# Optimization experiments

Hardware: AMD Instinct MI355X
Metric: run time of the kernel (lower is better)

## Reference

```python
import jax, jax.numpy as jnp
import numpy as np

N_NODES = 100000
N_EDGES = 1600000
IN_C = 128
HID = 128
OUT_C = 10
N_GRAPHS = 512


def setup_inputs() -> dict:
    key = jax.random.key(0)
    ks = jax.random.split(key, 12)
    x = jax.random.normal(ks[0], (N_NODES, IN_C), dtype=jnp.float32)
    edge_index = jax.random.randint(ks[1], (2, N_EDGES), 0, N_NODES, dtype=jnp.int64)
    batch = jnp.sort(jax.random.randint(ks[2], (N_NODES,), 0, N_GRAPHS, dtype=jnp.int64))

    def lin(k, fan_in, fan_out):
        bound = 1.0 / np.sqrt(fan_in)
        return jax.random.uniform(k, (fan_in, fan_out), jnp.float32, -bound, bound)

    params = {
        # GraphConv layer i: W_rel (neighbor aggregate transform, with bias),
        # W_root (self transform, no bias) -- matches PyG GraphConv.
        "W1_rel": lin(ks[3], IN_C, HID), "b1": jnp.zeros((HID,), jnp.float32), "W1_root": lin(ks[4], IN_C, HID),
        "W2_rel": lin(ks[5], HID, HID), "b2": jnp.zeros((HID,), jnp.float32), "W2_root": lin(ks[6], HID, HID),
        "W3_rel": lin(ks[7], HID, HID), "b3": jnp.zeros((HID,), jnp.float32), "W3_root": lin(ks[8], HID, HID),
        "W_lin": lin(ks[9], HID, OUT_C), "b_lin": jnp.zeros((OUT_C,), jnp.float32),
    }
    return {"x": x, "edge_index": edge_index, "batch": batch, **params}


def _graph_conv(x, src, dst, W_rel, b, W_root):
    # PyG GraphConv with aggr='add': out_i = W_rel @ sum_{j->i} x_j + b + W_root @ x_i
    agg = jax.ops.segment_sum(x[src], dst, num_segments=x.shape[0])  # [N, d]
    return agg @ W_rel + b + x @ W_root


def reference(x, edge_index, batch,
              W1_rel, b1, W1_root,
              W2_rel, b2, W2_root,
              W3_rel, b3, W3_root,
              W_lin, b_lin):
    src, dst = edge_index[0], edge_index[1]
    h = jax.nn.relu(_graph_conv(x, src, dst, W1_rel, b1, W1_root))
    h = jax.nn.relu(_graph_conv(h, src, dst, W2_rel, b2, W2_root))
    h = _graph_conv(h, src, dst, W3_rel, b3, W3_root)
    # global mean pool over graphs
    sums = jax.ops.segment_sum(h, batch, num_segments=N_GRAPHS)             # [G, d]
    counts = jax.ops.segment_sum(jnp.ones((h.shape[0],), h.dtype), batch, num_segments=N_GRAPHS)
    pooled = sums / jnp.maximum(counts, 1.0)[:, None]
    return pooled @ W_lin + b_lin  # [G, OUT_C]
```

## Files before the change

### kernel.cpp

```cpp
#include <hip/hip_runtime.h>

static constexpr int NN = 100000;
static constexpr int NE = 1600000;
static constexpr int C  = 128;
static constexpr int OC = 10;
static constexpr int NG = 512;

static constexpr int BSH  = 9;
static constexpr int BNW  = 1 << BSH;
static constexpr int BK   = (NN + BNW - 1) / BNW;
static constexpr int BCAP = 12288;
static constexpr int EPB  = 4096;
static constexpr int ABLK = (NE + EPB - 1) / EPB;

static constexpr int TSTRIDE = 132;
static constexpr int NSPLIT = 8;

static constexpr int PB_PACK = BK;
static constexpr int PB_GB   = PB_PACK + 16;
static constexpr int PB_WF   = PB_GB + 2;
static constexpr int PB_CVT  = PB_WF + 5;
static constexpr int PB_TOT  = PB_CVT + (NN * C / 8 + 511) / 512;

typedef unsigned short u16;
typedef __attribute__((ext_vector_type(8))) short short8;
typedef __attribute__((ext_vector_type(8))) short bf16x8;
typedef __attribute__((ext_vector_type(4))) float f32x4;

__device__ __forceinline__ float bf2f(u16 u) {
    union { float f; unsigned int u32; } v; v.u32 = ((unsigned int)u) << 16; return v.f;
}
__device__ __forceinline__ u16 f2bf(float f) {
    union { float f; unsigned int u; } v; v.f = f;
    unsigned int u = v.u;
    unsigned int r = u + 0x7FFF + ((u >> 16) & 1);
    return (u16)(r >> 16);
}

__global__ __launch_bounds__(256) void k_binA(const int* __restrict__ src,
                                              const int* __restrict__ dst,
                                              int* __restrict__ gcnt,
                                              int* __restrict__ buck) {
    __shared__ int cnt[BK];
    __shared__ int curs[BK];
    int tid = threadIdx.x;
    for (int i = tid; i < BK; i += 256) cnt[i] = 0;
    __syncthreads();
    int e0 = blockIdx.x * EPB;
    for (int i = tid; i < EPB; i += 256) {
        int e = e0 + i;
        if (e < NE) atomicAdd(&cnt[dst[e] >> BSH], 1);
    }
    __syncthreads();
    for (int i = tid; i < BK; i += 256) {
        int c = cnt[i];
        int gb = (c > 0) ? atomicAdd(&gcnt[i], c) : 0;
        curs[i] = i * BCAP + gb;
    }
    __syncthreads();
    for (int i = tid; i < EPB; i += 256) {
        int e = e0 + i;
        if (e < NE) {
            int d = dst[e];
            int b = d >> BSH;
            int p = atomicAdd(&curs[b], 1);
            if (p < (b + 1) * BCAP)
                buck[p] = (src[e] << BSH) | (d & (BNW - 1));
        }
    }
}

__global__ __launch_bounds__(512) void k_binbprep(
    const int* __restrict__ gcnt, const int* __restrict__ buck,
    int* __restrict__ rp, int* __restrict__ csr,
    const float* __restrict__ x, u16* __restrict__ xb,
    const float* __restrict__ W1r, const float* __restrict__ W1o,
    const float* __restrict__ W2r, const float* __restrict__ W2o,
    u16* __restrict__ Bp,
    const int* __restrict__ batch, int* __restrict__ gstart,
    const float* __restrict__ W3r, const float* __restrict__ W3o,
    const float* __restrict__ b3, const float* __restrict__ W_lin,
    const float* __restrict__ b_lin,
    float* __restrict__ Wrl, float* __restrict__ Wro, float* __restrict__ bfold) {
    int bid = blockIdx.x;
    int tid = threadIdx.x;

    if (bid < BK) {
        __shared__ int hist[BNW];
        __shared__ int scanbuf[BNW];
        int b = bid;

        scanbuf[tid] = (tid < b) ? gcnt[tid] : 0;
        __syncthreads();
        for (int off = 1; off < BNW; off <<= 1) {
            int t = (tid >= off) ? scanbuf[tid - off] : 0;
            __syncthreads();
            scanbuf[tid] += t;
            __syncthreads();
        }
        int base = scanbuf[BNW - 1];

        int n = gcnt[b];
        if (n > BCAP) n = BCAP;
        const int* bb = buck + (size_t)b * BCAP;

        hist[tid] = 0;
        __syncthreads();
        for (int i = tid; i < n; i += BNW) atomicAdd(&hist[bb[i] & (BNW - 1)], 1);
        __syncthreads();

        int v = hist[tid];
        scanbuf[tid] = v;
        __syncthreads();
        for (int off = 1; off < BNW; off <<= 1) {
            int t = (tid >= off) ? scanbuf[tid - off] : 0;
            __syncthreads();
            scanbuf[tid] += t;
            __syncthreads();
        }
        int excl = scanbuf[tid] - v;
        int node = (b << BSH) + tid;
        if (node < NN) rp[node] = base + excl;
        if (b == 0 && tid == 0) rp[NN] = NE;
        __syncthreads();
        hist[tid] = base + excl;
        __syncthreads();
        for (int i = tid; i < n; i += BNW) {
            int en = bb[i];
            int p = atomicAdd(&hist[en & (BNW - 1)], 1);
            csr[p] = en >> BSH;
        }
    } else if (bid < PB_GB) {
        int tt = (bid - PB_PACK) * 512 + tid;
        int layer = tt >> 12;
        int t = tt & 4095;
        const float* Wr = (layer == 0) ? W1r : W2r;
        const float* Wo = (layer == 0) ? W1o : W2o;
        u16* outp = Bp + layer * 32768;
        int lane = t & 63;
        int nfrag = (t >> 6) & 7;
        int kk = t >> 9;
        int col = nfrag * 16 + (lane & 15);
        int k0 = kk * 32 + (lane >> 4) * 8;
        u16 vals[8];
#pragma unroll
        for (int j = 0; j < 8; ++j) {
            int k = k0 + j;
            float w = (k < C) ? Wr[k * C + col] : Wo[(k - C) * C + col];
            vals[j] = f2bf(w);
        }
        *reinterpret_cast<short8*>(outp + (size_t)t * 8) = *reinterpret_cast<const short8*>(vals);
    } else if (bid < PB_WF) {
        int g = (bid - PB_GB) * 512 + tid;
        if (g > NG) return;
        int lo = 0, hi = NN;
        while (lo < hi) { int mid = (lo + hi) >> 1; if (batch[mid] < g) lo = mid + 1; else hi = mid; }
        gstart[g] = lo;
    } else if (bid < PB_CVT) {
        int idx = (bid - PB_WF) * 512 + tid;
        if (idx >= OC * 256) return;
        int o = idx >> 8;
        int sub = idx & 255;
        if (sub < 128) {
            float s = 0.0f;
#pragma unroll 8
            for (int c = 0; c < C; ++c) s += W3r[sub * C + c] * W_lin[c * OC + o];
            Wrl[sub * OC + o] = s;
        } else {
            int k = sub - 128;
            float s = 0.0f;
#pragma unroll 8
            for (int c = 0; c < C; ++c) s += W3o[k * C + c] * W_lin[c * OC + o];
            Wro[k * OC + o] = s;
        }
        if (sub == 0) {
            float s = 0.0f;
            for (int c = 0; c < C; ++c) s += b3[c] * W_lin[c * OC + o];
            bfold[o] = b_lin[o] + s;
        }
    } else {
        int i = (bid - PB_CVT) * 512 + tid;
        size_t base = (size_t)i * 8;
        if (base >= (size_t)NN * C) return;
        float4 a = *reinterpret_cast<const float4*>(x + base);
        float4 b = *reinterpret_cast<const float4*>(x + base + 4);
        u16 o[8] = { f2bf(a.x), f2bf(a.y), f2bf(a.z), f2bf(a.w),
                     f2bf(b.x), f2bf(b.y), f2bf(b.z), f2bf(b.w) };
        *reinterpret_cast<short8*>(xb + base) = *reinterpret_cast<const short8*>(o);
    }
}

__global__ __launch_bounds__(256) void k_gather(const u16* __restrict__ h,
                                                const int* __restrict__ rp,
                                                const int* __restrict__ csr,
                                                u16* __restrict__ agg) {
    int t = blockIdx.x * blockDim.x + threadIdx.x;
    int node = t >> 6;
    if (node >= NN) return;
    int lane = t & 63;
    int jj = lane >> 4;
    int seg = (lane & 15) * 8;
    int beg = rp[node], end = rp[node + 1];

    float acc[8] = {};
    int j0 = beg;
    for (; j0 + 8 <= end; j0 += 8) {
        int sa = csr[j0 + jj];
        int sb = csr[j0 + 4 + jj];
        short8 va = *reinterpret_cast<const short8*>(h + (size_t)sa * C + seg);
        short8 vb = *reinterpret_cast<const short8*>(h + (size_t)sb * C + seg);
#pragma unroll
        for (int q = 0; q < 8; ++q) {
            acc[q] += bf2f((u16)va[q]);
            acc[q] += bf2f((u16)vb[q]);
        }
    }
    if (j0 < end) {
        int ja = j0 + jj;
        int jb = j0 + 4 + jj;
        if (ja < end) {
            int sa = csr[ja];
            short8 va = *reinterpret_cast<const short8*>(h + (size_t)sa * C + seg);
#pragma unroll
            for (int q = 0; q < 8; ++q) acc[q] += bf2f((u16)va[q]);
        }
        if (jb < end) {
            int sb = csr[jb];
            short8 vb = *reinterpret_cast<const short8*>(h + (size_t)sb * C + seg);
#pragma unroll
            for (int q = 0; q < 8; ++q) acc[q] += bf2f((u16)vb[q]);
        }
    }

#pragma unroll
    for (int q = 0; q < 8; ++q) {
        acc[q] += __shfl_xor(acc[q], 32);
        acc[q] += __shfl_xor(acc[q], 16);
    }
    if (lane < 16) {
        u16 o[8];
#pragma unroll
        for (int q = 0; q < 8; ++q) o[q] = f2bf(acc[q]);
        *reinterpret_cast<short8*>(agg + (size_t)node * C + seg) =
            *reinterpret_cast<const short8*>(o);
    }
}

template <bool RELU, bool TSUM>
__global__ __launch_bounds__(256) void k_transform_mfma(
    const u16* __restrict__ agg, const u16* __restrict__ h,
    const u16* __restrict__ Bp, const float* __restrict__ bias,
    u16* __restrict__ out,
    const int* __restrict__ batch, float* __restrict__ Tpart) {
    __shared__ u16 tile[4][16 * TSTRIDE];
    int wave = threadIdx.x >> 6;
    int lane = threadIdx.x & 63;
    int row0 = blockIdx.x * 64 + wave * 16;
    int arow = row0 + (lane & 15);
    int rclamp = arow < NN ? arow : NN - 1;
    int koff = (lane >> 4) * 8;

    bf16x8 afr[8];
#pragma unroll
    for (int kk = 0; kk < 4; ++kk)
        afr[kk] = *reinterpret_cast<const bf16x8*>(agg + (size_t)rclamp * C + kk * 32 + koff);
#pragma unroll
    for (int kk = 0; kk < 4; ++kk)
        afr[4 + kk] = *reinterpret_cast<const bf16x8*>(h + (size_t)rclamp * C + kk * 32 + koff);

    f32x4 acc[8] = {};
#pragma unroll
    for (int kk = 0; kk < 8; ++kk) {
        const u16* bp = Bp + ((size_t)kk * 8 * 64 + lane) * 8;
#pragma unroll
        for (int n = 0; n < 8; ++n) {
            bf16x8 b = *reinterpret_cast<const bf16x8*>(bp + (size_t)n * 64 * 8);
            acc[n] = __builtin_amdgcn_mfma_f32_16x16x32_bf16(afr[kk], b, acc[n], 0, 0, 0);
        }
    }

    u16* T = tile[wave];
    int colbase = lane & 15;
    int rloc = (lane >> 4) * 4;
#pragma unroll
    for (int n = 0; n < 8; ++n) {
        int col = n * 16 + colbase;
        float bb = bias[col];
#pragma unroll
        for (int r = 0; r < 4; ++r) {
            float v = acc[n][r] + bb;
            if (RELU) v = fmaxf(v, 0.0f);
            T[(rloc + r) * TSTRIDE + col] = f2bf(v);
        }
    }
    __syncthreads();

#pragma unroll
    for (int k = 0; k < 4; ++k) {
        int idx = k * 64 + lane;
        int lr = idx >> 4;
        int off = (idx & 15) * 8;
        int ro = row0 + lr;
        if (ro < NN) {
            short8 v = *reinterpret_cast<const short8*>(&T[lr * TSTRIDE + off]);
            *reinterpret_cast<short8*>(out + (size_t)ro * C + off) = v;
        }
    }

    if (TSUM) {
        if (threadIdx.x < C) {
            int c = threadIdx.x;
            int base = blockIdx.x * 64;
            float run = 0.0f;
            int curg = -1;
            for (int r = 0; r < 64; ++r) {
                int ro = base + r;
                if (ro >= NN) break;
                int g = batch[ro];
                if (g != curg) {
                    if (curg >= 0) atomicAdd(&Tpart[(size_t)curg * C + c], run);
                    run = 0.0f;
                    curg = g;
                }
                run += bf2f(tile[r >> 4][(r & 15) * TSTRIDE + c]);
            }
            if (curg >= 0) atomicAdd(&Tpart[(size_t)curg * C + c], run);
        }
    }
}

__global__ __launch_bounds__(256) void k_gsum(
    const u16* __restrict__ h, const int* __restrict__ rp,
    const int* __restrict__ csr, const int* __restrict__ gstart,
    float* __restrict__ partial) {
    int b = blockIdx.x;
    int g = b >> 3;
    int p = b & 7;
    int slot = threadIdx.x >> 4;
    int seg = (threadIdx.x & 15) * 8;

    int gs = gstart[g], ge = gstart[g + 1];
    int es = rp[gs], ee = rp[ge];
    int m = ee - es;
    int js = es + (int)(((long long)m * p) >> 3);
    int je = es + (int)(((long long)m * (p + 1)) >> 3);

    float acc[8] = {};
    int j = js + slot;
    for (; j + 48 < je; j += 64) {
        int r0 = csr[j];
        int r1 = csr[j + 16];
        int r2 = csr[j + 32];
        int r3 = csr[j + 48];
        short8 v0 = *reinterpret_cast<const short8*>(h + (size_t)r0 * C + seg);
        short8 v1 = *reinterpret_cast<const short8*>(h + (size_t)r1 * C + seg);
        short8 v2 = *reinterpret_cast<const short8*>(h + (size_t)r2 * C + seg);
        short8 v3 = *reinterpret_cast<const short8*>(h + (size_t)r3 * C + seg);
#pragma unroll
        for (int q = 0; q < 8; ++q) {
            acc[q] += bf2f((u16)v0[q]);
            acc[q] += bf2f((u16)v1[q]);
            acc[q] += bf2f((u16)v2[q]);
            acc[q] += bf2f((u16)v3[q]);
        }
    }
    for (; j < je; j += 16) {
        int r0 = csr[j];
        short8 v0 = *reinterpret_cast<const short8*>(h + (size_t)r0 * C + seg);
#pragma unroll
        for (int q = 0; q < 8; ++q) acc[q] += bf2f((u16)v0[q]);
    }

    __shared__ float red[16][C];
#pragma unroll
    for (int q = 0; q < 8; ++q) red[slot][seg + q] = acc[q];
    __syncthreads();
    if (threadIdx.x < C) {
        float s = 0.0f;
#pragma unroll
        for (int r = 0; r < 16; ++r) s += red[r][threadIdx.x];
        partial[(size_t)b * C + threadIdx.x] = s;
    }
}

__global__ __launch_bounds__(128) void k_gout(
    const float* __restrict__ partial, const float* __restrict__ Tpart,
    const int* __restrict__ gstart,
    const float* __restrict__ Wrl, const float* __restrict__ Wro,
    const float* __restrict__ bfold, float* __restrict__ out) {
    int g = blockIdx.x;
    int k = threadIdx.x;
    __shared__ float S[C], T[C];
    float s = 0.0f;
#pragma unroll
    for (int p = 0; p < NSPLIT; ++p)
        s += partial[((size_t)(g * NSPLIT + p)) * C + k];
    S[k] = s;
    T[k] = Tpart[(size_t)g * C + k];
    __syncthreads();
    if (k < OC) {
        int n = gstart[g + 1] - gstart[g];
        float inv = 1.0f / (float)max(n, 1);
        float o = bfold[k];
#pragma unroll 8
        for (int kk = 0; kk < C; ++kk)
            o += (S[kk] * Wrl[kk * OC + k] + T[kk] * Wro[kk * OC + k]) * inv;
        out[g * OC + k] = o;
    }
}

extern "C" void kernel_launch(void* const* d_in, const int* in_sizes, int n_in,
                              void* d_out, int out_size, void* d_ws, size_t ws_size,
                              hipStream_t stream) {
    const float* x       = (const float*)d_in[0];
    const int*   eidx    = (const int*)d_in[1];
    const int*   batch   = (const int*)d_in[2];
    const float* W1_rel  = (const float*)d_in[3];
    const float* b1      = (const float*)d_in[4];
    const float* W1_root = (const float*)d_in[5];
    const float* W2_rel  = (const float*)d_in[6];
    const float* b2      = (const float*)d_in[7];
    const float* W2_root = (const float*)d_in[8];
    const float* W3_rel  = (const float*)d_in[9];
    const float* b3      = (const float*)d_in[10];
    const float* W3_root = (const float*)d_in[11];
    const float* W_lin   = (const float*)d_in[12];
    const float* b_lin   = (const float*)d_in[13];
    float* out = (float*)d_out;

    const int* src = eidx;
    const int* dst = eidx + NE;

    u16* xb   = (u16*)d_ws;
    u16* hb   = xb + (size_t)NN * C;
    u16* aggb = hb + (size_t)NN * C;
    u16* Bp   = aggb + (size_t)NN * C;
    int* rp      = (int*)(Bp + 2 * 32768);
    int* csr     = rp + NN + 1;
    int* buck    = csr + NE;
    int* gcnt    = buck + (size_t)BK * BCAP;
    float* Tpart = (float*)(gcnt + BK);
    int* gstart  = (int*)(Tpart + (size_t)NG * C);
    float* partial = (float*)(gstart + NG + 2);
    float* Wrl   = partial + (size_t)NG * NSPLIT * C;
    float* Wro   = Wrl + C * OC;
    float* bfold = Wro + C * OC;

    const int gb = (NN * 64 + 255) / 256;
    const int tb = (NN + 63) / 64;

    hipMemsetAsync(gcnt, 0, BK * sizeof(int) + (size_t)NG * C * sizeof(float), stream);
    k_binA<<<ABLK, 256, 0, stream>>>(src, dst, gcnt, buck);

    k_binbprep<<<PB_TOT, 512, 0, stream>>>(gcnt, buck, rp, csr,
                                           x, xb, W1_rel, W1_root, W2_rel, W2_root,
                                           Bp, batch, gstart,
                                           W3_rel, W3_root, b3, W_lin, b_lin,
                                           Wrl, Wro, bfold);

    k_gather<<<gb, 256, 0, stream>>>(xb, rp, csr, aggb);
    k_transform_mfma<true, false><<<tb, 256, 0, stream>>>(aggb, xb, Bp, b1, hb,
                                                          batch, Tpart);

    k_gather<<<gb, 256, 0, stream>>>(hb, rp, csr, aggb);
    k_transform_mfma<true, true><<<tb, 256, 0, stream>>>(aggb, hb, Bp + 32768, b2,
                                                         hb, batch, Tpart);

    k_gsum<<<NG * NSPLIT, 256, 0, stream>>>(hb, rp, csr, gstart, partial);
    k_gout<<<NG, 128, 0, stream>>>(partial, Tpart, gstart, Wrl, Wro, bfold, out);
}
```

Baseline: 294.8 us.

## Regroup prep kernels, stage weight fragments in LDS, fuse graph output into gsum

Moves the weight packing, x-to-bf16 conversion and graph-start search into the edge-binning kernel, and runs the CSR build as its own kernel. The MFMA transform now double-buffers the packed weight fragments through shared memory instead of reading them from global memory per wave. The final per-graph projection is folded into the gsum kernel using a last-block atomic counter, which removes one launch. This adds extra barriers in the transform loop and a fence-plus-atomic step at the end of every gsum block.

Result: slower. 899.1 us (+205.0%).

```diff
diff --git a/kernel.cpp b/kernel.cpp
--- a/kernel.cpp
+++ b/kernel.cpp
@@ -16,11 +16,11 @@
 static constexpr int TSTRIDE = 132;
 static constexpr int NSPLIT = 8;
 
-static constexpr int PB_PACK = BK;
-static constexpr int PB_GB   = PB_PACK + 16;
-static constexpr int PB_WF   = PB_GB + 2;
-static constexpr int PB_CVT  = PB_WF + 5;
-static constexpr int PB_TOT  = PB_CVT + (NN * C / 8 + 511) / 512;
+static constexpr int APB_PACK = ABLK;
+static constexpr int APB_GB   = APB_PACK + 32;
+static constexpr int APB_WF   = APB_GB + 3;
+static constexpr int APB_CVT  = APB_WF + 10;
+static constexpr int APB_TOT  = APB_CVT + (NN * C / 8 + 255) / 256;
 
 typedef unsigned short u16;
 typedef __attribute__((ext_vector_type(8))) short short8;
@@ -37,42 +37,9 @@
     return (u16)(r >> 16);
 }
 
-__global__ __launch_bounds__(256) void k_binA(const int* __restrict__ src,
-                                              const int* __restrict__ dst,
-                                              int* __restrict__ gcnt,
-                                              int* __restrict__ buck) {
-    __shared__ int cnt[BK];
-    __shared__ int curs[BK];
-    int tid = threadIdx.x;
-    for (int i = tid; i < BK; i += 256) cnt[i] = 0;
-    __syncthreads();
-    int e0 = blockIdx.x * EPB;
-    for (int i = tid; i < EPB; i += 256) {
-        int e = e0 + i;
-        if (e < NE) atomicAdd(&cnt[dst[e] >> BSH], 1);
-    }
-    __syncthreads();
-    for (int i = tid; i < BK; i += 256) {
-        int c = cnt[i];
-        int gb = (c > 0) ? atomicAdd(&gcnt[i], c) : 0;
-        curs[i] = i * BCAP + gb;
-    }
-    __syncthreads();
-    for (int i = tid; i < EPB; i += 256) {
-        int e = e0 + i;
-        if (e < NE) {
-            int d = dst[e];
-            int b = d >> BSH;
-            int p = atomicAdd(&curs[b], 1);
-            if (p < (b + 1) * BCAP)
-                buck[p] = (src[e] << BSH) | (d & (BNW - 1));
-        }
-    }
-}
-
-__global__ __launch_bounds__(512) void k_binbprep(
-    const int* __restrict__ gcnt, const int* __restrict__ buck,
-    int* __restrict__ rp, int* __restrict__ csr,
+__global__ __launch_bounds__(256) void k_binA_prep(
+    const int* __restrict__ src, const int* __restrict__ dst,
+    int* __restrict__ gcnt, int* __restrict__ buck,
     const float* __restrict__ x, u16* __restrict__ xb,
     const float* __restrict__ W1r, const float* __restrict__ W1o,
     const float* __restrict__ W2r, const float* __restrict__ W2o,
@@ -85,53 +52,35 @@
     int bid = blockIdx.x;
     int tid = threadIdx.x;
 
-    if (bid < BK) {
-        __shared__ int hist[BNW];
-        __shared__ int scanbuf[BNW];
-        int b = bid;
-
-        scanbuf[tid] = (tid < b) ? gcnt[tid] : 0;
-        __syncthreads();
-        for (int off = 1; off < BNW; off <<= 1) {
-            int t = (tid >= off) ? scanbuf[tid - off] : 0;
-            __syncthreads();
-            scanbuf[tid] += t;
-            __syncthreads();
-        }
-        int base = scanbuf[BNW - 1];
-
-        int n = gcnt[b];
-        if (n > BCAP) n = BCAP;
-        const int* bb = buck + (size_t)b * BCAP;
-
-        hist[tid] = 0;
-        __syncthreads();
-        for (int i = tid; i < n; i += BNW) atomicAdd(&hist[bb[i] & (BNW - 1)], 1);
-        __syncthreads();
-
-        int v = hist[tid];
-        scanbuf[tid] = v;
-        __syncthreads();
-        for (int off = 1; off < BNW; off <<= 1) {
-            int t = (tid >= off) ? scanbuf[tid - off] : 0;
-            __syncthreads();
-            scanbuf[tid] += t;
-            __syncthreads();
-        }
-        int excl = scanbuf[tid] - v;
-        int node = (b << BSH) + tid;
-        if (node < NN) rp[node] = base + excl;
-        if (b == 0 && tid == 0) rp[NN] = NE;
-        __syncthreads();
-        hist[tid] = base + excl;
-        __syncthreads();
-        for (int i = tid; i < n; i += BNW) {
-            int en = bb[i];
-            int p = atomicAdd(&hist[en & (BNW - 1)], 1);
-            csr[p] = en >> BSH;
-        }
-    } else if (bid < PB_GB) {
-        int tt = (bid - PB_PACK) * 512 + tid;
+    if (bid < ABLK) {
+        __shared__ int cnt[BK];
+        __shared__ int curs[BK];
+        for (int i = tid; i < BK; i += 256) cnt[i] = 0;
+        __syncthreads();
+        int e0 = bid * EPB;
+        for (int i = tid; i < EPB; i += 256) {
+            int e = e0 + i;
+            if (e < NE) atomicAdd(&cnt[dst[e] >> BSH], 1);
+        }
+        __syncthreads();
+        for (int i = tid; i < BK; i += 256) {
+            int c = cnt[i];
+            int gb = (c > 0) ? atomicAdd(&gcnt[i], c) : 0;
+            curs[i] = i * BCAP + gb;
+        }
+        __syncthreads();
+        for (int i = tid; i < EPB; i += 256) {
+            int e = e0 + i;
+            if (e < NE) {
+                int d = dst[e];
+                int b = d >> BSH;
+                int p = atomicAdd(&curs[b], 1);
+                if (p < (b + 1) * BCAP)
+                    buck[p] = (src[e] << BSH) | (d & (BNW - 1));
+            }
+        }
+    } else if (bid < APB_GB) {
+        int tt = (bid - APB_PACK) * 256 + tid;
         int layer = tt >> 12;
         int t = tt & 4095;
         const float* Wr = (layer == 0) ? W1r : W2r;
@@ -150,14 +99,14 @@
             vals[j] = f2bf(w);
         }
         *reinterpret_cast<short8*>(outp + (size_t)t * 8) = *reinterpret_cast<const short8*>(vals);
-    } else if (bid < PB_WF) {
-        int g = (bid - PB_GB) * 512 + tid;
+    } else if (bid < APB_WF) {
+        int g = (bid - APB_GB) * 256 + tid;
         if (g > NG) return;
         int lo = 0, hi = NN;
         while (lo < hi) { int mid = (lo + hi) >> 1; if (batch[mid] < g) lo = mid + 1; else hi = mid; }
         gstart[g] = lo;
-    } else if (bid < PB_CVT) {
-        int idx = (bid - PB_WF) * 512 + tid;
+    } else if (bid < APB_CVT) {
+        int idx = (bid - APB_WF) * 256 + tid;
         if (idx >= OC * 256) return;
         int o = idx >> 8;
         int sub = idx & 255;
@@ -179,7 +128,7 @@
             bfold[o] = b_lin[o] + s;
         }
     } else {
-        int i = (bid - PB_CVT) * 512 + tid;
+        int i = (bid - APB_CVT) * 256 + tid;
         size_t base = (size_t)i * 8;
         if (base >= (size_t)NN * C) return;
         float4 a = *reinterpret_cast<const float4*>(x + base);
@@ -187,6 +136,57 @@
         u16 o[8] = { f2bf(a.x), f2bf(a.y), f2bf(a.z), f2bf(a.w),
                      f2bf(b.x), f2bf(b.y), f2bf(b.z), f2bf(b.w) };
         *reinterpret_cast<short8*>(xb + base) = *reinterpret_cast<const short8*>(o);
+    }
+}
+
+__global__ __launch_bounds__(BNW) void k_binB(const int* __restrict__ gcnt,
+                                              const int* __restrict__ buck,
+                                              int* __restrict__ rp,
+                                              int* __restrict__ csr) {
+    int b = blockIdx.x;
+    int tid = threadIdx.x;
+    __shared__ int hist[BNW];
+    __shared__ int scanbuf[BNW];
+
+    scanbuf[tid] = (tid < b) ? gcnt[tid] : 0;
+    __syncthreads();
+    for (int off = 1; off < BNW; off <<= 1) {
+        int t = (tid >= off) ? scanbuf[tid - off] : 0;
+        __syncthreads();
+        scanbuf[tid] += t;
+        __syncthreads();
+    }
+    int base = scanbuf[BNW - 1];
+
+    int n = gcnt[b];
+    if (n > BCAP) n = BCAP;
+    const int* bb = buck + (size_t)b * BCAP;
+
+    hist[tid] = 0;
+    __syncthreads();
+    for (int i = tid; i < n; i += BNW) atomicAdd(&hist[bb[i] & (BNW - 1)], 1);
+    __syncthreads();
+
+    int v = hist[tid];
+    scanbuf[tid] = v;
+    __syncthreads();
+    for (int off = 1; off < BNW; off <<= 1) {
+        int t = (tid >= off) ? scanbuf[tid - off] : 0;
+        __syncthreads();
+        scanbuf[tid] += t;
+        __syncthreads();
+    }
+    int excl = scanbuf[tid] - v;
+    int node = (b << BSH) + tid;
+    if (node < NN) rp[node] = base + excl;
+    if (b == 0 && tid == 0) rp[NN] = NE;
+    __syncthreads();
+    hist[tid] = base + excl;
+    __syncthreads();
+    for (int i = tid; i < n; i += BNW) {
+        int en = bb[i];
+        int p = atomicAdd(&hist[en & (BNW - 1)], 1);
+        csr[p] = en >> BSH;
     }
 }
 
@@ -253,13 +253,22 @@
     u16* __restrict__ out,
     const int* __restrict__ batch, float* __restrict__ Tpart) {
     __shared__ u16 tile[4][16 * TSTRIDE];
-    int wave = threadIdx.x >> 6;
-    int lane = threadIdx.x & 63;
+    __shared__ u16 bsl[2][4096];
+    int tid = threadIdx.x;
+    int wave = tid >> 6;
+    int lane = tid & 63;
     int row0 = blockIdx.x * 64 + wave * 16;
     int arow = row0 + (lane & 15);
     int rclamp = arow < NN ? arow : NN - 1;
     int koff = (lane >> 4) * 8;
 
+    {
+        const short8* sp = reinterpret_cast<const short8*>(Bp);
+        short8* dp = reinterpret_cast<short8*>(bsl[0]);
+        dp[tid] = sp[tid];
+        dp[tid + 256] = sp[tid + 256];
+    }
+
     bf16x8 afr[8];
 #pragma unroll
     for (int kk = 0; kk < 4; ++kk)
@@ -271,10 +280,17 @@
     f32x4 acc[8] = {};
 #pragma unroll
     for (int kk = 0; kk < 8; ++kk) {
-        const u16* bp = Bp + ((size_t)kk * 8 * 64 + lane) * 8;
+        __syncthreads();
+        if (kk < 7) {
+            const short8* sp = reinterpret_cast<const short8*>(Bp + (size_t)(kk + 1) * 4096);
+            short8* dp = reinterpret_cast<short8*>(bsl[(kk + 1) & 1]);
+            dp[tid] = sp[tid];
+            dp[tid + 256] = sp[tid + 256];
+        }
+        const u16* bp = &bsl[kk & 1][lane * 8];
 #pragma unroll
         for (int n = 0; n < 8; ++n) {
-            bf16x8 b = *reinterpret_cast<const bf16x8*>(bp + (size_t)n * 64 * 8);
+            bf16x8 b = *reinterpret_cast<const bf16x8*>(bp + n * 64 * 8);
             acc[n] = __builtin_amdgcn_mfma_f32_16x16x32_bf16(afr[kk], b, acc[n], 0, 0, 0);
         }
     }
@@ -308,8 +324,8 @@
     }
 
     if (TSUM) {
-        if (threadIdx.x < C) {
-            int c = threadIdx.x;
+        if (tid < C) {
+            int c = tid;
             int base = blockIdx.x * 64;
             float run = 0.0f;
             int curg = -1;
@@ -329,15 +345,19 @@
     }
 }
 
-__global__ __launch_bounds__(256) void k_gsum(
+__global__ __launch_bounds__(256) void k_gsum_out(
     const u16* __restrict__ h, const int* __restrict__ rp,
     const int* __restrict__ csr, const int* __restrict__ gstart,
-    float* __restrict__ partial) {
+    float* __restrict__ partial, const float* __restrict__ Tpart,
+    const float* __restrict__ Wrl, const float* __restrict__ Wro,
+    const float* __restrict__ bfold, int* __restrict__ gcount,
+    float* __restrict__ out) {
     int b = blockIdx.x;
     int g = b >> 3;
     int p = b & 7;
-    int slot = threadIdx.x >> 4;
-    int seg = (threadIdx.x & 15) * 8;
+    int tid = threadIdx.x;
+    int slot = tid >> 4;
+    int seg = (tid & 15) * 8;
 
     int gs = gstart[g], ge = gstart[g + 1];
     int es = rp[gs], ee = rp[ge];
@@ -375,37 +395,38 @@
 #pragma unroll
     for (int q = 0; q < 8; ++q) red[slot][seg + q] = acc[q];
     __syncthreads();
-    if (threadIdx.x < C) {
+    if (tid < C) {
         float s = 0.0f;
 #pragma unroll
-        for (int r = 0; r < 16; ++r) s += red[r][threadIdx.x];
-        partial[(size_t)b * C + threadIdx.x] = s;
-    }
-}
-
-__global__ __launch_bounds__(128) void k_gout(
-    const float* __restrict__ partial, const float* __restrict__ Tpart,
-    const int* __restrict__ gstart,
-    const float* __restrict__ Wrl, const float* __restrict__ Wro,
-    const float* __restrict__ bfold, float* __restrict__ out) {
-    int g = blockIdx.x;
-    int k = threadIdx.x;
+        for (int r = 0; r < 16; ++r) s += red[r][tid];
+        partial[(size_t)b * C + tid] = s;
+    }
+
+    __threadfence();
+    __shared__ int last;
+    if (tid == 0) last = (atomicAdd(&gcount[g], 1) == NSPLIT - 1) ? 1 : 0;
+    __syncthreads();
+    if (!last) return;
+    __threadfence();
+
     __shared__ float S[C], T[C];
-    float s = 0.0f;
-#pragma unroll
-    for (int p = 0; p < NSPLIT; ++p)
-        s += partial[((size_t)(g * NSPLIT + p)) * C + k];
-    S[k] = s;
-    T[k] = Tpart[(size_t)g * C + k];
-    __syncthreads();
-    if (k < OC) {
-        int n = gstart[g + 1] - gstart[g];
+    if (tid < C) {
+        float s = 0.0f;
+#pragma unroll
+        for (int q = 0; q < NSPLIT; ++q)
+            s += partial[((size_t)(g * NSPLIT + q)) * C + tid];
+        S[tid] = s;
+        T[tid] = Tpart[(size_t)g * C + tid];
+    }
+    __syncthreads();
+    if (tid < OC) {
+        int n = ge - gs;
         float inv = 1.0f / (float)max(n, 1);
-        float o = bfold[k];
+        float o = bfold[tid];
 #pragma unroll 8
         for (int kk = 0; kk < C; ++kk)
-            o += (S[kk] * Wrl[kk * OC + k] + T[kk] * Wro[kk * OC + k]) * inv;
-        out[g * OC + k] = o;
+            o += (S[kk] * Wrl[kk * OC + tid] + T[kk] * Wro[kk * OC + tid]) * inv;
+        out[g * OC + tid] = o;
     }
 }
 
@@ -439,7 +460,8 @@
     int* csr     = rp + NN + 1;
     int* buck    = csr + NE;
     int* gcnt    = buck + (size_t)BK * BCAP;
-    float* Tpart = (float*)(gcnt + BK);
+    int* gcount  = gcnt + BK;
+    float* Tpart = (float*)(gcount + NG);
     int* gstart  = (int*)(Tpart + (size_t)NG * C);
     float* partial = (float*)(gstart + NG + 2);
     float* Wrl   = partial + (size_t)NG * NSPLIT * C;
@@ -449,14 +471,16 @@
     const int gb = (NN * 64 + 255) / 256;
     const int tb = (NN + 63) / 64;
 
-    hipMemsetAsync(gcnt, 0, BK * sizeof(int) + (size_t)NG * C * sizeof(float), stream);
-    k_binA<<<ABLK, 256, 0, stream>>>(src, dst, gcnt, buck);
-
-    k_binbprep<<<PB_TOT, 512, 0, stream>>>(gcnt, buck, rp, csr,
-                                           x, xb, W1_rel, W1_root, W2_rel, W2_root,
-                                           Bp, batch, gstart,
-                                           W3_rel, W3_root, b3, W_lin, b_lin,
-                                           Wrl, Wro, bfold);
+    hipMemsetAsync(gcnt, 0, (BK + NG) * sizeof(int) + (size_t)NG * C * sizeof(float),
+                   stream);
+
+    k_binA_prep<<<APB_TOT, 256, 0, stream>>>(src, dst, gcnt, buck,
+                                             x, xb, W1_rel, W1_root, W2_rel, W2_root,
+                                             Bp, batch, gstart,
+                                             W3_rel, W3_root, b3, W_lin, b_lin,
+                                             Wrl, Wro, bfold);
+
+    k_binB<<<BK, BNW, 0, stream>>>(gcnt, buck, rp, csr);
 
     k_gather<<<gb, 256, 0, stream>>>(xb, rp, csr, aggb);
     k_transform_mfma<true, false><<<tb, 256, 0, stream>>>(aggb, xb, Bp, b1, hb,
@@ -466,6 +490,6 @@
     k_transform_mfma<true, true><<<tb, 256, 0, stream>>>(aggb, hb, Bp + 32768, b2,
                                                          hb, batch, Tpart);
 
-    k_gsum<<<NG * NSPLIT, 256, 0, stream>>>(hb, rp, csr, gstart, partial);
-    k_gout<<<NG, 128, 0, stream>>>(partial, Tpart, gstart, Wrl, Wro, bfold, out);
-}
+    k_gsum_out<<<NG * NSPLIT, 256, 0, stream>>>(hb, rp, csr, gstart, partial,
+                                                Tpart, Wrl, Wro, bfold, gcount, out);
+}
```
